# Optimization experiments

Measured on AMD Instinct MI355X. Metric: run time of the kernel, lower is better.

Reference implementation:

```python
import jax, jax.numpy as jnp
import numpy as np

DIM = 1024
EPS = 1e-5


def setup_inputs() -> dict:
    key = jax.random.key(0)
    ks = jax.random.split(key, 7)
    C = DIM
    x = jax.random.normal(ks[0], (4, 4096, C), dtype=jnp.float32)
    norm_w = jnp.ones((C,), dtype=jnp.float32)
    norm_b = jnp.zeros((C,), dtype=jnp.float32)
    s = 1.0 / np.sqrt(C)
    qkv_w = jax.random.uniform(ks[1], (3 * C, C), dtype=jnp.float32, minval=-s, maxval=s)
    qkv_b = jax.random.uniform(ks[2], (3 * C,), dtype=jnp.float32, minval=-s, maxval=s)
    proj_w = jax.random.uniform(ks[3], (C, C), dtype=jnp.float32, minval=-s, maxval=s)
    proj_b = jax.random.uniform(ks[4], (C,), dtype=jnp.float32, minval=-s, maxval=s)
    return {"x": x, "norm_w": norm_w, "norm_b": norm_b, "qkv_w": qkv_w,
            "qkv_b": qkv_b, "proj_w": proj_w, "proj_b": proj_b}


def _layernorm(x, w, b):
    mu = jnp.mean(x, axis=-1, keepdims=True)
    var = jnp.mean(jnp.square(x - mu), axis=-1, keepdims=True)
    return (x - mu) * jax.lax.rsqrt(var + EPS) * w + b


def reference(x, norm_w, norm_b, qkv_w, qkv_b, proj_w, proj_b):
    B, T, C = x.shape
    residual = x
    h = _layernorm(x, norm_w, norm_b)
    qkv = jnp.einsum('btc,oc->bto', h, qkv_w) + qkv_b  # [B,T,3C]
    q, k, v = qkv[..., :C], qkv[..., C:2 * C], qkv[..., 2 * C:]
    attn = jnp.einsum('btc,bsc->bts', q, k) / jnp.sqrt(jnp.float32(C))  # raw QK^T, no softmax
    o = jnp.einsum('bts,bsc->btc', attn, v)
    o = jnp.einsum('btc,oc->bto', o, proj_w) + proj_b
    return residual + o  # dropout is identity in eval mode
```

## Files before the change

kernel.cpp:

```cpp
#include <hip/hip_runtime.h>

typedef _Float16 f16;
typedef _Float16 f16x4 __attribute__((ext_vector_type(4)));
typedef _Float16 f16x8 __attribute__((ext_vector_type(8)));
typedef float f32x4 __attribute__((ext_vector_type(4)));

#define AS1 __attribute__((address_space(1)))
#define AS3 __attribute__((address_space(3)))

__device__ __forceinline__ void gl_lds16(const f16* g, f16* l) {
  __builtin_amdgcn_global_load_lds((const AS1 void*)g, (AS3 void*)l, 16, 0, 0);
}

__global__ __launch_bounds__(256) void ln_kernel(const float* __restrict__ x,
                                                 const float* __restrict__ gw,
                                                 const float* __restrict__ gb,
                                                 f16* __restrict__ H) {
  const int wv = threadIdx.x >> 6, lane = threadIdx.x & 63;
  const long row = (long)blockIdx.x * 4 + wv;
  const float* xr = x + row * 1024;
  float4 v[4];
  float s = 0.f, s2 = 0.f;
#pragma unroll
  for (int j = 0; j < 4; ++j) {
    v[j] = ((const float4*)xr)[lane + 64 * j];
    s  += v[j].x + v[j].y + v[j].z + v[j].w;
    s2 += v[j].x * v[j].x + v[j].y * v[j].y + v[j].z * v[j].z + v[j].w * v[j].w;
  }
#pragma unroll
  for (int off = 32; off > 0; off >>= 1) {
    s  += __shfl_xor(s, off);
    s2 += __shfl_xor(s2, off);
  }
  const float mu = s * (1.0f / 1024.0f);
  const float rstd = rsqrtf(s2 * (1.0f / 1024.0f) - mu * mu + 1e-5f);
#pragma unroll
  for (int j = 0; j < 4; ++j) {
    const float4 w4 = ((const float4*)gw)[lane + 64 * j];
    const float4 b4 = ((const float4*)gb)[lane + 64 * j];
    f16x4 h;
    h[0] = (f16)((v[j].x - mu) * rstd * w4.x + b4.x);
    h[1] = (f16)((v[j].y - mu) * rstd * w4.y + b4.y);
    h[2] = (f16)((v[j].z - mu) * rstd * w4.z + b4.z);
    h[3] = (f16)((v[j].w - mu) * rstd * w4.w + b4.w);
    *(f16x4*)(H + row * 1024 + (lane + 64 * j) * 4) = h;
  }
}

__global__ __launch_bounds__(256) void transpose_cs_kernel(const f16* __restrict__ H,
                                                           f16* __restrict__ Ht,
                                                           float* __restrict__ hs) {
  __shared__ f16 tile[64][68];
  __shared__ float csum[4][64];
  const int b = blockIdx.z;
  const long Hb  = (long)b * 4096 * 1024;
  const long Htb = (long)b * 1024 * 4096;
  const int t0 = blockIdx.y * 64, c0 = blockIdx.x * 64;
  const int tid = threadIdx.x;
  const int r = tid >> 2, g0 = tid & 3;
#pragma unroll
  for (int i = 0; i < 4; ++i) {
    const int g = g0 + i * 4;
    f16x4 v = *(const f16x4*)(H + Hb + (long)(t0 + r) * 1024 + c0 + g * 4);
    *(f16x4*)&tile[r][g * 4] = v;
  }
  __syncthreads();
  {
    const int cl = tid & 63, rg = tid >> 6;
    float s = 0.f;
#pragma unroll
    for (int rr = 0; rr < 16; ++rr) s += (float)tile[rg * 16 + rr][cl];
    csum[rg][cl] = s;
  }
#pragma unroll
  for (int i = 0; i < 4; ++i) {
    const int g = g0 + i * 4;
    f16x4 v;
    v[0] = tile[g * 4 + 0][r];
    v[1] = tile[g * 4 + 1][r];
    v[2] = tile[g * 4 + 2][r];
    v[3] = tile[g * 4 + 3][r];
    *(f16x4*)(Ht + Htb + (long)(c0 + r) * 4096 + t0 + g * 4) = v;
  }
  __syncthreads();
  if (tid < 64)
    atomicAdd(&hs[b * 1024 + c0 + tid],
              csum[0][tid] + csum[1][tid] + csum[2][tid] + csum[3][tid]);
}

__global__ __launch_bounds__(256) void transcast4(const float* __restrict__ qkv_w,
                                                  const float* __restrict__ proj_w,
                                                  f16* __restrict__ WT3,
                                                  f16* __restrict__ Wh,
                                                  f16* __restrict__ Ph) {
  const int z = blockIdx.z;
  __shared__ f16 tile[64][68];
  const int r0 = blockIdx.y * 64, c0 = blockIdx.x * 64;
  const int tid = threadIdx.x;
  const int r = tid >> 2, g0 = tid & 3;
  if (z == 3) {
#pragma unroll
    for (int i = 0; i < 4; ++i) {
      const int g = g0 + i * 4;
      float4 v = *(const float4*)(proj_w + (long)(r0 + r) * 1024 + c0 + g * 4);
      f16x4 h; h[0]=(f16)v.x; h[1]=(f16)v.y; h[2]=(f16)v.z; h[3]=(f16)v.w;
      *(f16x4*)(Ph + (long)(r0 + r) * 1024 + c0 + g * 4) = h;
    }
    return;
  }
  const float* W = qkv_w + (long)z * 1048576;
  f16* WT = WT3 + (long)z * 1048576;
#pragma unroll
  for (int i = 0; i < 4; ++i) {
    const int g = g0 + i * 4;
    float4 v = *(const float4*)(W + (long)(r0 + r) * 1024 + c0 + g * 4);
    f16x4 h; h[0]=(f16)v.x; h[1]=(f16)v.y; h[2]=(f16)v.z; h[3]=(f16)v.w;
    *(f16x4*)&tile[r][g * 4] = h;
    if (z >= 1)
      *(f16x4*)(Wh + (long)z * 1048576 + (long)(r0 + r) * 1024 + c0 + g * 4) = h;
  }
  __syncthreads();
#pragma unroll
  for (int i = 0; i < 4; ++i) {
    const int g = g0 + i * 4;
    f16x4 v;
    v[0] = tile[g * 4 + 0][r];
    v[1] = tile[g * 4 + 1][r];
    v[2] = tile[g * 4 + 2][r];
    v[3] = tile[g * 4 + 3][r];
    *(f16x4*)(WT + (long)(c0 + r) * 1024 + r0 + g * 4) = v;
  }
}

__device__ __forceinline__ float dot1024(const f16* __restrict__ row,
                                         const float* __restrict__ v) {
  const int lane = threadIdx.x & 63;
  float s = 0.f;
#pragma unroll
  for (int j = 0; j < 2; ++j) {
    const int d = (lane + 64 * j) * 8;
    f16x8 a = *(const f16x8*)(row + d);
    float4 h0 = *(const float4*)(v + d);
    float4 h1 = *(const float4*)(v + d + 4);
    s += (float)a[0] * h0.x + (float)a[1] * h0.y + (float)a[2] * h0.z + (float)a[3] * h0.w
       + (float)a[4] * h1.x + (float)a[5] * h1.y + (float)a[6] * h1.z + (float)a[7] * h1.w;
  }
#pragma unroll
  for (int off = 32; off > 0; off >>= 1) s += __shfl_down(s, off);
  return s;
}

__device__ __forceinline__ float dotf1024(const float* __restrict__ a,
                                          const float* __restrict__ v) {
  const int lane = threadIdx.x & 63;
  float s = 0.f;
#pragma unroll
  for (int j = 0; j < 4; ++j) {
    const int d = (lane + 64 * j) * 4;
    float4 x = *(const float4*)(a + d);
    float4 q = *(const float4*)(v + d);
    s += x.x * q.x + x.y * q.y + x.z * q.z + x.w * q.w;
  }
#pragma unroll
  for (int off = 32; off > 0; off >>= 1) s += __shfl_down(s, off);
  return s;
}

__global__ void gemv3a(const f16* __restrict__ WT3, const f16* __restrict__ Ph,
                       const float* __restrict__ qkv_b, float* __restrict__ ayd,
                       float* __restrict__ scal) {
  if (blockIdx.x == 3072) {
    float s = dotf1024(qkv_b + 1024, qkv_b);
    if ((threadIdx.x & 63) == 0) scal[4] = s;
    return;
  }
  const int which = blockIdx.x >> 10, m = blockIdx.x & 1023;
  const f16* row;
  const float* v;
  if (which == 0)      { row = WT3 + (long)m * 1024;            v = qkv_b + 1024; }
  else if (which == 1) { row = WT3 + 1048576 + (long)m * 1024;  v = qkv_b; }
  else                 { row = Ph + (long)m * 1024;             v = qkv_b + 2048; }
  float s = dot1024(row, v);
  if ((threadIdx.x & 63) == 0) ayd[which * 1024 + m] = s;
}

__global__ void gemv_uw2(const f16* __restrict__ Wh, const float* __restrict__ hs,
                         const float* __restrict__ ayd,
                         float* __restrict__ wvec, float* __restrict__ scal) {
  const int bid = blockIdx.x;
  if (bid >= 4096) {
    const int b = bid - 4096;
    float s = dotf1024(hs + b * 1024, ayd + 1024);
    if ((threadIdx.x & 63) == 0) scal[b] = s;
    return;
  }
  const int b = bid >> 10, i = bid & 1023;
  float s = dot1024(Wh + (long)(2048 + i) * 1024, hs + b * 1024);
  if ((threadIdx.x & 63) == 0) wvec[b * 1024 + i] = s;
}

__global__ void gemv3b(const f16* __restrict__ U, const f16* __restrict__ PWv,
                       const f16* __restrict__ Gh, const float* __restrict__ hs,
                       const float* __restrict__ ayd, float* __restrict__ efz) {
  const int sel = blockIdx.x >> 12, r = blockIdx.x & 4095;
  const int b = r >> 10, m = r & 1023;
  const f16* row;
  const float* v;
  if (sel == 0)      { row = U + (long)m * 1024;                       v = hs + b * 1024; }
  else if (sel == 1) { row = PWv + (long)m * 1024;                     v = hs + b * 1024; }
  else               { row = Gh + (long)b * 1048576 + (long)m * 1024;  v = ayd + 1024; }
  float s = dot1024(row, v);
  if ((threadIdx.x & 63) == 0) efz[sel * 4096 + r] = s;
}

__global__ void gemvW(const f16* __restrict__ Wh, const float* __restrict__ efz,
                      const float* __restrict__ qkv_b, const float* __restrict__ scal,
                      const float* __restrict__ wvec, float* __restrict__ w1) {
  const int b = blockIdx.x >> 10, i = blockIdx.x & 1023;
  float s = dot1024(Wh + (long)(2048 + i) * 1024, efz + 8192 + b * 1024);
  if ((threadIdx.x & 63) == 0) {
    const float bv = qkv_b[2048 + i];
    w1[b * 1024 + i] = (s + bv * scal[b] + scal[4] * (wvec[b * 1024 + i] + 4096.f * bv)) * 0.03125f;
  }
}

__global__ void gemvC2(const f16* __restrict__ Ph, const float* __restrict__ w1,
                       const float* __restrict__ proj_b, float* __restrict__ c2) {
  const int b = blockIdx.x >> 10, c = blockIdx.x & 1023;
  float s = dot1024(Ph + (long)c * 1024, w1 + b * 1024);
  if ((threadIdx.x & 63) == 0) c2[b * 1024 + c] = s + proj_b[c];
}

#define GP64_COMMON()                                        \
  const int tid = threadIdx.x;                               \
  const int wave = tid >> 6, lane = tid & 63;                \
  const int lr = lane & 15, lk = lane >> 4;                  \
  const int srow = tid >> 3;                                 \
  const int slc  = (tid & 7) ^ (srow & 7);                   \
  const int kc0 = ((lk) ^ (lr & 7)) * 8;                     \
  const int kc1 = ((4 + lk) ^ (lr & 7)) * 8;

#define GEMM_WAIT8(NBUF_, r_)                                               \
  do {                                                                      \
    if constexpr (NBUF_ == 3) {                                             \
      if ((r_) >= 2)      asm volatile("s_waitcnt vmcnt(16)" ::: "memory"); \
      else if ((r_) == 1) asm volatile("s_waitcnt vmcnt(8)" ::: "memory");  \
      else                asm volatile("s_waitcnt vmcnt(0)" ::: "memory");  \
    } else {                                                                \
      if ((r_) >= 1)      asm volatile("s_waitcnt vmcnt(8)" ::: "memory");  \
      else                asm volatile("s_waitcnt vmcnt(0)" ::: "memory");  \
    }                                                                       \
  } while (0)

#define COMP64_HALF(asb_, bsb_, kc_)                                             \
  do {                                                                           \
    const f16* asb = (asb_);                                                     \
    const f16* bsb = (bsb_);                                                     \
    f16x8 af[4], bf[4];                                                          \
    _Pragma("unroll")                                                            \
    for (int mi = 0; mi < 4; ++mi)                                               \
      af[mi] = *(const f16x8*)(asb + (wm * 64 + mi * 16 + lr) * 64 + (kc_));     \
    _Pragma("unroll")                                                            \
    for (int ni = 0; ni < 4; ++ni)                                               \
      bf[ni] = *(const f16x8*)(bsb + (wn * 64 + ni * 16 + lr) * 64 + (kc_));     \
    _Pragma("unroll")                                                            \
    for (int mi = 0; mi < 4; ++mi)                                               \
      _Pragma("unroll")                                                          \
      for (int ni = 0; ni < 4; ++ni)                                             \
        acc[mi][ni] = __builtin_amdgcn_mfma_f32_16x16x32_f16(af[mi], bf[ni],     \
                                                             acc[mi][ni], 0, 0, 0); \
  } while (0)

#define GEMM_BODY_LOOP(NBUF_, NT_, STAGEM)                       \
  do {                                                           \
    if constexpr (NBUF_ == 3) {                                  \
      STAGEM(0, 0); STAGEM(1, 1);                                \
      int cur = 0, stg = 2;                                      \
      for (int t = 0; t < (NT_); ++t) {                          \
        if (t + 2 < (NT_)) STAGEM(stg, t + 2);                   \
        GEMM_WAIT8(3, (NT_) - 1 - t);                            \
        asm volatile("s_barrier" ::: "memory");                  \
        __builtin_amdgcn_s_setprio(1);                           \
        COMP64_HALF(&As[cur][0], &Bs[cur][0], kc0);              \
        COMP64_HALF(&As[cur][0], &Bs[cur][0], kc1);              \
        __builtin_amdgcn_s_setprio(0);                           \
        asm volatile("s_waitcnt lgkmcnt(0)" ::: "memory");       \
        asm volatile("s_barrier" ::: "memory");                  \
        cur = (cur + 1 == 3) ? 0 : cur + 1;                      \
        stg = (stg + 1 == 3) ? 0 : stg + 1;                      \
      }                                                          \
    } else {                                                     \
      STAGEM(0, 0);                                              \
      int cur = 0;                                               \
      for (int t = 0; t < (NT_); ++t) {                          \
        if (t + 1 < (NT_)) STAGEM(cur ^ 1, t + 1);               \
        GEMM_WAIT8(2, (NT_) - 1 - t);                            \
        asm volatile("s_barrier" ::: "memory");                  \
        __builtin_amdgcn_s_setprio(1);                           \
        COMP64_HALF(&As[cur][0], &Bs[cur][0], kc0);              \
        COMP64_HALF(&As[cur][0], &Bs[cur][0], kc1);              \
        __builtin_amdgcn_s_setprio(0);                           \
        asm volatile("s_waitcnt lgkmcnt(0)" ::: "memory");       \
        asm volatile("s_barrier" ::: "memory");                  \
        cur ^= 1;                                                \
      }                                                          \
    }                                                            \
  } while (0)

template <int MODE>
__global__ __launch_bounds__(256) void gemm128(
    const f16* __restrict__ A, const f16* __restrict__ B, int K,
    long sA, long sB, long sC,
    f16* __restrict__ Ch,
    const float* __restrict__ dvec, const float* __restrict__ evec,
    const float* __restrict__ fvec, const float* __restrict__ avec) {
  const int b = blockIdx.z;
  A += (long)b * sA;
  B += (long)b * sB;
  const int nx = blockIdx.y & 7;
  const int ny = blockIdx.x;

  GP64_COMMON();
  const int wm = wave >> 1, wn = wave & 1;

  __shared__ __align__(16) f16 As[3][8192];
  __shared__ __align__(16) f16 Bs[3][8192];

  const long aoffs = (long)(ny * 128 + srow) * K + slc * 8;
  const long boffs = (long)(nx * 128 + srow) * K + slc * 8;

  f32x4 zero = {0.f, 0.f, 0.f, 0.f};
  f32x4 acc[4][4];
#pragma unroll
  for (int mi = 0; mi < 4; ++mi)
#pragma unroll
    for (int ni = 0; ni < 4; ++ni) acc[mi][ni] = zero;

#define STAGE(buf, kt)                                                              \
  do {                                                                              \
    f16* asb = &As[buf][0];                                                         \
    f16* bsb = &Bs[buf][0];                                                         \
    _Pragma("unroll")                                                               \
    for (int q = 0; q < 4; ++q) {                                                   \
      gl_lds16(A + aoffs + (long)q * 32 * K + (kt) * 64, asb + q * 2048 + tid * 8); \
      gl_lds16(B + boffs + (long)q * 32 * K + (kt) * 64, bsb + q * 2048 + tid * 8); \
    }                                                                               \
  } while (0)

  const int nt = K >> 6;
  GEMM_BODY_LOOP(3, nt, STAGE);
#undef STAGE

  const long cb = (long)b * sC;
  const int m0 = ny * 128 + wm * 64;
  const int n0 = nx * 128 + wn * 64;
#pragma unroll
  for (int mi = 0; mi < 4; ++mi)
#pragma unroll
    for (int ni = 0; ni < 4; ++ni)
#pragma unroll
      for (int j = 0; j < 4; ++j) {
        const int gm = m0 + mi * 16 + lk * 4 + j;
        const int gn = n0 + ni * 16 + lr;
        float val = acc[mi][ni][j];
        if constexpr (MODE == 0) {
          Ch[cb + (long)gm * 1024 + gn] = (f16)val;
        } else {
          const float dm = dvec[gm];
          const float fm = fvec[b * 1024 + gm];
          const float en = evec[b * 1024 + gn];
          const float an = avec[gn];
          val = (val + dm * en + (fm + 4096.f * dm) * an) * 0.03125f;
          Ch[cb + (long)gm * 1024 + gn] = (f16)val;
        }
      }
}

__global__ __launch_bounds__(256) void gemmGUV(const f16* __restrict__ Ht,
                                               const f16* __restrict__ WT3,
                                               const f16* __restrict__ Ph,
                                               f16* __restrict__ part,
                                               f16* __restrict__ U,
                                               f16* __restrict__ PWv) {
  GP64_COMMON();
  const int wm = wave >> 1, wn = wave & 1;

  __shared__ __align__(16) f16 As[2][8192];
  __shared__ __align__(16) f16 Bs[2][8192];

  const int bid = blockIdx.x;
  const f16 *Ab, *Bb;
  long rs;
  int tileid = 0, zz = 0, selt = 0;
  if (bid < 576) {
    tileid = bid % 36;
    zz = bid / 36;
    const int b = zz & 3, ks4 = zz >> 2;
    int ti = 0, trem = tileid;
    while (trem >= 8 - ti) { trem -= 8 - ti; ++ti; }
    const int tj = ti + trem;
    const f16* Hb = Ht + (long)b * 4194304;
    rs = 4096;
    Ab = Hb + (long)(ti * 128 + srow) * 4096 + (long)ks4 * 1024 + slc * 8;
    Bb = Hb + (long)(tj * 128 + srow) * 4096 + (long)ks4 * 1024 + slc * 8;
  } else {
    const int u = bid - 576;
    selt = (u >> 6) + 1;
    const int t = u & 63;
    const int ny = t >> 3, nxx = t & 7;
    const f16* A0 = (selt == 2) ? Ph : WT3;
    const f16* B0 = (selt == 2) ? (WT3 + 2097152) : (WT3 + 1048576);
    rs = 1024;
    Ab = A0 + (long)(ny * 128 + srow) * 1024 + slc * 8;
    Bb = B0 + (long)(nxx * 128 + srow) * 1024 + slc * 8;
  }

  f32x4 zero = {0.f, 0.f, 0.f, 0.f};
  f32x4 acc[4][4];
#pragma unroll
  for (int mi = 0; mi < 4; ++mi)
#pragma unroll
    for (int ni = 0; ni < 4; ++ni) acc[mi][ni] = zero;

#define STAGE(buf, kt)                                                            \
  do {                                                                            \
    f16* asb = &As[buf][0];                                                       \
    f16* bsb = &Bs[buf][0];                                                       \
    _Pragma("unroll")                                                             \
    for (int q = 0; q < 4; ++q) {                                                 \
      gl_lds16(Ab + (long)q * 32 * rs + (kt) * 64, asb + q * 2048 + tid * 8);     \
      gl_lds16(Bb + (long)q * 32 * rs + (kt) * 64, bsb + q * 2048 + tid * 8);     \
    }                                                                             \
  } while (0)

  GEMM_BODY_LOOP(2, 16, STAGE);
#undef STAGE

  if (selt == 0) {
    f16* P = part + ((long)zz * 36 + tileid) * 16384;
#pragma unroll
    for (int mi = 0; mi < 4; ++mi)
#pragma unroll
      for (int ni = 0; ni < 4; ++ni)
#pragma unroll
        for (int j = 0; j < 4; ++j) {
          const int gm = wm * 64 + mi * 16 + lk * 4 + j;
          const int gn = wn * 64 + ni * 16 + lr;
          P[gm * 128 + gn] = (f16)acc[mi][ni][j];
        }
  } else {
    const int u = bid - 576;
    const int t = u & 63;
    const int ny = t >> 3, nxx = t & 7;
    f16* C = (selt == 2) ? PWv : U;
    const int m0 = ny * 128 + wm * 64;
    const int n0 = nxx * 128 + wn * 64;
#pragma unroll
    for (int mi = 0; mi < 4; ++mi)
#pragma unroll
      for (int ni = 0; ni < 4; ++ni)
#pragma unroll
        for (int j = 0; j < 4; ++j) {
          const int gm = m0 + mi * 16 + lk * 4 + j;
          const int gn = n0 + ni * 16 + lr;
          C[(long)gm * 1024 + gn] = (f16)acc[mi][ni][j];
        }
  }
}

__global__ __launch_bounds__(512) void gemm256f(
    const f16* __restrict__ A,
    const f16* __restrict__ Bw,
    const float* __restrict__ resid,
    const float* __restrict__ c2v,
    float* __restrict__ outF) {
  const int lin = blockIdx.y * 4 + blockIdx.x;
  const int xcd = lin & 7, slot = lin >> 3;
  const int ny = xcd * 8 + (slot >> 2);
  const int nx = slot & 3;
  const int bb = ny >> 4;

  GP64_COMMON();
  const int wm = wave >> 2, wn = wave & 3;

  __shared__ __align__(16) f16 As[2][16384];
  __shared__ __align__(16) f16 Bs[2][16384];

  const f16* Ab = A + (long)ny * 262144;
  const f16* Bb = Bw + (long)bb * 1048576 + (long)nx * 262144;
  const long offs = (long)srow * 1024 + slc * 8;

  f32x4 zero = {0.f, 0.f, 0.f, 0.f};
  f32x4 acc[8][4];
#pragma unroll
  for (int mi = 0; mi < 8; ++mi)
#pragma unroll
    for (int ni = 0; ni < 4; ++ni) acc[mi][ni] = zero;

#define STAGE(buf, kt)                                                             \
  do {                                                                             \
    f16* asb = &As[buf][0];                                                        \
    f16* bsb = &Bs[buf][0];                                                        \
    _Pragma("unroll")                                                              \
    for (int q = 0; q < 4; ++q) {                                                  \
      gl_lds16(Ab + offs + (long)q * 65536 + (kt) * 64, asb + q * 4096 + tid * 8); \
      gl_lds16(Bb + offs + (long)q * 65536 + (kt) * 64, bsb + q * 4096 + tid * 8); \
    }                                                                              \
  } while (0)

  const int nt = 16;
  STAGE(0, 0);
  int cur = 0;
  for (int t = 0; t < nt; ++t) {
    if (t + 1 < nt) STAGE(cur ^ 1, t + 1);
    GEMM_WAIT8(2, nt - 1 - t);
    asm volatile("s_barrier" ::: "memory");
    __builtin_amdgcn_s_setprio(1);
#pragma unroll
    for (int ks = 0; ks < 2; ++ks) {
      const int kc = ks ? kc1 : kc0;
      const f16* asb = &As[cur][0];
      const f16* bsb = &Bs[cur][0];
      f16x8 af[8], bf[4];
#pragma unroll
      for (int mi = 0; mi < 8; ++mi)
        af[mi] = *(const f16x8*)(asb + (wm * 128 + mi * 16 + lr) * 64 + kc);
#pragma unroll
      for (int ni = 0; ni < 4; ++ni)
        bf[ni] = *(const f16x8*)(bsb + (wn * 64 + ni * 16 + lr) * 64 + kc);
#pragma unroll
      for (int mi = 0; mi < 8; ++mi)
#pragma unroll
        for (int ni = 0; ni < 4; ++ni)
          acc[mi][ni] = __builtin_amdgcn_mfma_f32_16x16x32_f16(af[mi], bf[ni],
                                                               acc[mi][ni], 0, 0, 0);
    }
    __builtin_amdgcn_s_setprio(0);
    asm volatile("s_waitcnt lgkmcnt(0)" ::: "memory");
    asm volatile("s_barrier" ::: "memory");
    cur ^= 1;
  }
#undef STAGE

  float* weps = ((float*)&As[0][0]) + wave * 1088;
  const int m0 = ny * 256 + wm * 128;
  const int n0 = nx * 256 + wn * 64;
  const int err = lane >> 3;
  const int ecc = (lane & 7) * 4;
  float4 cc2[2];
#pragma unroll
  for (int q = 0; q < 2; ++q)
    cc2[q] = *(const float4*)&c2v[bb * 1024 + n0 + ecc + 32 * q];

  float4 rb0[4], rb1[4];

#define RESLD(DST, MI)                                                            \
  do {                                                                            \
    _Pragma("unroll")                                                             \
    for (int h = 0; h < 2; ++h)                                                   \
      _Pragma("unroll")                                                           \
      for (int q = 0; q < 2; ++q)                                                 \
        DST[h * 2 + q] = *(const float4*)&resid[                                  \
            (long)(m0 + (MI) * 16 + err + 8 * h) * 1024 + n0 + ecc + 32 * q];     \
  } while (0)

#define EPI(MI, CUR, NXT, LASTP)                                                  \
  do {                                                                            \
    _Pragma("unroll")                                                             \
    for (int ni = 0; ni < 4; ++ni)                                                \
      _Pragma("unroll")                                                           \
      for (int j = 0; j < 4; ++j)                                                 \
        weps[(lk * 4 + j) * 68 + ni * 16 + lr] = acc[MI][ni][j];                  \
    if (!(LASTP)) RESLD(NXT, (MI) + 1);                                           \
    asm volatile("s_waitcnt lgkmcnt(0)" ::: "memory");                            \
    _Pragma("unroll")                                                             \
    for (int h = 0; h < 2; ++h)                                                   \
      _Pragma("unroll")                                                           \
      for (int q = 0; q < 2; ++q) {                                               \
        const int rr = err + 8 * h;                                               \
        const int cc = ecc + 32 * q;                                              \
        float4 o = *(const float4*)&weps[rr * 68 + cc];                           \
        const long gbase = (long)(m0 + (MI) * 16 + rr) * 1024 + n0 + cc;          \
        const float4 rv = CUR[h * 2 + q];                                         \
        float4 ov;                                                               \
        ov.x = o.x + rv.x + cc2[q].x;                                             \
        ov.y = o.y + rv.y + cc2[q].y;                                             \
        ov.z = o.z + rv.z + cc2[q].z;                                             \
        ov.w = o.w + rv.w + cc2[q].w;                                             \
        *(float4*)&outF[gbase] = ov;                                              \
      }                                                                           \
  } while (0)

  RESLD(rb0, 0);
  EPI(0, rb0, rb1, 0);
  EPI(1, rb1, rb0, 0);
  EPI(2, rb0, rb1, 0);
  EPI(3, rb1, rb0, 0);
  EPI(4, rb0, rb1, 0);
  EPI(5, rb1, rb0, 0);
  EPI(6, rb0, rb1, 0);
  EPI(7, rb1, rb0, 1);
#undef RESLD
#undef EPI
}

__global__ __launch_bounds__(256) void treduce(const f16* __restrict__ part,
                                               f16* __restrict__ Gh) {
  const int tileid = blockIdx.x, b = blockIdx.y;
  int ti = 0, trem = tileid;
  while (trem >= 8 - ti) { trem -= 8 - ti; ++ti; }
  const int tj = ti + trem;
  __shared__ f16 tl[128][132];
  const int tid = threadIdx.x;
  f16* Gb = Gh + (long)b * 1048576;
  const long pbase = ((long)b * 36 + tileid) * 16384;
#pragma unroll
  for (int it = 0; it < 16; ++it) {
    const int e = it * 1024 + tid * 4;
    const int r = e >> 7, c = e & 127;
    f16x4 p0 = *(const f16x4*)(part + pbase + e);
    f16x4 p1 = *(const f16x4*)(part + pbase + 2359296 + e);
    f16x4 p2 = *(const f16x4*)(part + pbase + 4718592 + e);
    f16x4 p3 = *(const f16x4*)(part + pbase + 7077888 + e);
    f16x4 sv;
#pragma unroll
    for (int j = 0; j < 4; ++j)
      sv[j] = (f16)((float)p0[j] + (float)p1[j] + (float)p2[j] + (float)p3[j]);
    *(f16x4*)(Gb + (long)(ti * 128 + r) * 1024 + tj * 128 + c) = sv;
    *(f16x4*)&tl[r][c] = sv;
  }
  if (ti != tj) {
    __syncthreads();
#pragma unroll
    for (int it = 0; it < 16; ++it) {
      const int e = it * 1024 + tid * 4;
      const int r = e >> 7, c = e & 127;
      f16x4 v;
      v[0] = tl[c + 0][r];
      v[1] = tl[c + 1][r];
      v[2] = tl[c + 2][r];
      v[3] = tl[c + 3][r];
      *(f16x4*)(Gb + (long)(tj * 128 + r) * 1024 + ti * 128 + c) = v;
    }
  }
}

extern "C" void kernel_launch(void* const* d_in, const int* in_sizes, int n_in,
                              void* d_out, int out_size, void* d_ws, size_t ws_size,
                              hipStream_t stream) {
  const float* x      = (const float*)d_in[0];
  const float* norm_w = (const float*)d_in[1];
  const float* norm_b = (const float*)d_in[2];
  const float* qkv_w  = (const float*)d_in[3];
  const float* qkv_b  = (const float*)d_in[4];
  const float* proj_w = (const float*)d_in[5];
  const float* proj_b = (const float*)d_in[6];
  float* out = (float*)d_out;
  char* ws = (char*)d_ws;

  const size_t OFF_H    = 0;
  const size_t OFF_HT   = 33554432;
  const size_t OFF_T1   = 33554432;
  const size_t OFF_T2   = 41943040;
  const size_t OFF_WH   = 67108864;
  const size_t OFF_PH   = 73400320;
  const size_t OFF_WT3  = 75497472;
  const size_t OFF_U    = 81788928;
  const size_t OFF_PWV  = 83886080;
  const size_t OFF_GH   = 85983232;
  const size_t OFF_PART = 94371840;
  const size_t OFF_HS   = 115343360;
  const size_t OFF_WVEC = 115376128;
  const size_t OFF_AYD  = 115392512;
  const size_t OFF_SCAL = 115404800;
  const size_t OFF_EFZ  = 115405824;
  const size_t OFF_W1   = 115454976;
  const size_t OFF_C2   = 115471360;

  f16* H    = (f16*)(ws + OFF_H);
  f16* Ht   = (f16*)(ws + OFF_HT);
  f16* T1   = (f16*)(ws + OFF_T1);
  f16* T2   = (f16*)(ws + OFF_T2);
  f16* Wh   = (f16*)(ws + OFF_WH);
  f16* Ph   = (f16*)(ws + OFF_PH);
  f16* WT3  = (f16*)(ws + OFF_WT3);
  f16* U    = (f16*)(ws + OFF_U);
  f16* PWv  = (f16*)(ws + OFF_PWV);
  f16* Gh   = (f16*)(ws + OFF_GH);
  f16* part = (f16*)(ws + OFF_PART);
  float* hs   = (float*)(ws + OFF_HS);
  float* wvec = (float*)(ws + OFF_WVEC);
  float* ayd  = (float*)(ws + OFF_AYD);
  float* scal = (float*)(ws + OFF_SCAL);
  float* efz  = (float*)(ws + OFF_EFZ);
  float* w1   = (float*)(ws + OFF_W1);
  float* c2v  = (float*)(ws + OFF_C2);

  transcast4<<<dim3(16, 16, 4), 256, 0, stream>>>(qkv_w, proj_w, WT3, Wh, Ph);
  gemv3a<<<dim3(3073), 64, 0, stream>>>(WT3, Ph, qkv_b, ayd, scal);

  ln_kernel<<<dim3(4096), 256, 0, stream>>>(x, norm_w, norm_b, H);
  hipMemsetAsync(ws + OFF_HS, 0, 16384, stream);
  transpose_cs_kernel<<<dim3(16, 64, 4), 256, 0, stream>>>(H, Ht, hs);
  gemv_uw2<<<dim3(4100), 64, 0, stream>>>(Wh, hs, ayd, wvec, scal);

  gemmGUV<<<dim3(704), 256, 0, stream>>>(Ht, WT3, Ph, part, U, PWv);
  treduce<<<dim3(36, 4), 256, 0, stream>>>(part, Gh);

  gemm128<0><<<dim3(8, 8, 4), 256, 0, stream>>>(U, Gh, 1024, 0L, 1048576L, 1048576L,
      T1, nullptr, nullptr, nullptr, nullptr);

  gemv3b<<<dim3(12288), 64, 0, stream>>>(U, PWv, Gh, hs, ayd, efz);
  gemvW<<<dim3(4096), 64, 0, stream>>>(Wh, efz, qkv_b, scal, wvec, w1);
  gemvC2<<<dim3(4096), 64, 0, stream>>>(Ph, w1, proj_b, c2v);

  gemm128<1><<<dim3(8, 8, 4), 256, 0, stream>>>(PWv, T1, 1024, 0L, 1048576L, 1048576L,
      T2, ayd + 2048, efz, efz + 4096, ayd);

  gemm256f<<<dim3(4, 64), 512, 0, stream>>>(H, T2, x, c2v, out);
}
```

Baseline: 208.7 us.

## Fold bias-correction GEMVs via PWv, split final GEMM MFMA phases

The bias-correction chain of three GEMVs (wvec through Wh, w1 through Wh, c2 through Ph) is replaced by one GEMV over the precomputed PWv product plus existing efz terms. The small scal dot products move into gemv3b, which removes two kernel launches and about two matrix-vector passes over 1024x1024 weights. The final gemm256f inner loop now splits the 8 M-fragments into two halves, each with its own LDS wait, priority raise and barrier. Its epilogue also drops the double-buffered residual prefetch in favour of a simpler loop. The extra barriers and the lost residual prefetch could cost time in the large final GEMM.

```diff
diff --git a/kernel.cpp b/kernel.cpp
--- a/kernel.cpp
+++ b/kernel.cpp
@@ -184,24 +184,16 @@
   if ((threadIdx.x & 63) == 0) ayd[which * 1024 + m] = s;
 }
 
-__global__ void gemv_uw2(const f16* __restrict__ Wh, const float* __restrict__ hs,
-                         const float* __restrict__ ayd,
-                         float* __restrict__ wvec, float* __restrict__ scal) {
-  const int bid = blockIdx.x;
-  if (bid >= 4096) {
-    const int b = bid - 4096;
+__global__ void gemv3b(const f16* __restrict__ U, const f16* __restrict__ PWv,
+                       const f16* __restrict__ Gh, const float* __restrict__ hs,
+                       const float* __restrict__ ayd, float* __restrict__ efz,
+                       float* __restrict__ scal) {
+  if (blockIdx.x >= 12288) {
+    const int b = blockIdx.x - 12288;
     float s = dotf1024(hs + b * 1024, ayd + 1024);
     if ((threadIdx.x & 63) == 0) scal[b] = s;
     return;
   }
-  const int b = bid >> 10, i = bid & 1023;
-  float s = dot1024(Wh + (long)(2048 + i) * 1024, hs + b * 1024);
-  if ((threadIdx.x & 63) == 0) wvec[b * 1024 + i] = s;
-}
-
-__global__ void gemv3b(const f16* __restrict__ U, const f16* __restrict__ PWv,
-                       const f16* __restrict__ Gh, const float* __restrict__ hs,
-                       const float* __restrict__ ayd, float* __restrict__ efz) {
   const int sel = blockIdx.x >> 12, r = blockIdx.x & 4095;
   const int b = r >> 10, m = r & 1023;
   const f16* row;
@@ -213,22 +205,16 @@
   if ((threadIdx.x & 63) == 0) efz[sel * 4096 + r] = s;
 }
 
-__global__ void gemvW(const f16* __restrict__ Wh, const float* __restrict__ efz,
-                      const float* __restrict__ qkv_b, const float* __restrict__ scal,
-                      const float* __restrict__ wvec, float* __restrict__ w1) {
-  const int b = blockIdx.x >> 10, i = blockIdx.x & 1023;
-  float s = dot1024(Wh + (long)(2048 + i) * 1024, efz + 8192 + b * 1024);
+__global__ void gemvC2n(const f16* __restrict__ PWv, const float* __restrict__ efz,
+                        const float* __restrict__ ayd, const float* __restrict__ scal,
+                        const float* __restrict__ proj_b, float* __restrict__ c2) {
+  const int b = blockIdx.x >> 10, c = blockIdx.x & 1023;
+  float s = dot1024(PWv + (long)c * 1024, efz + 8192 + b * 1024);
   if ((threadIdx.x & 63) == 0) {
-    const float bv = qkv_b[2048 + i];
-    w1[b * 1024 + i] = (s + bv * scal[b] + scal[4] * (wvec[b * 1024 + i] + 4096.f * bv)) * 0.03125f;
-  }
-}
-
-__global__ void gemvC2(const f16* __restrict__ Ph, const float* __restrict__ w1,
-                       const float* __restrict__ proj_b, float* __restrict__ c2) {
-  const int b = blockIdx.x >> 10, c = blockIdx.x & 1023;
-  float s = dot1024(Ph + (long)c * 1024, w1 + b * 1024);
-  if ((threadIdx.x & 63) == 0) c2[b * 1024 + c] = s + proj_b[c];
+    const float d = ayd[2048 + c];
+    c2[b * 1024 + c] = (s + d * scal[b] + scal[4] * (efz[4096 + b * 1024 + c] + 4096.f * d))
+                         * 0.03125f + proj_b[c];
+  }
 }
 
 #define GP64_COMMON()                                        \
@@ -515,29 +501,42 @@
     if (t + 1 < nt) STAGE(cur ^ 1, t + 1);
     GEMM_WAIT8(2, nt - 1 - t);
     asm volatile("s_barrier" ::: "memory");
-    __builtin_amdgcn_s_setprio(1);
+    const f16* asb = &As[cur][0];
+    const f16* bsb = &Bs[cur][0];
 #pragma unroll
     for (int ks = 0; ks < 2; ++ks) {
       const int kc = ks ? kc1 : kc0;
-      const f16* asb = &As[cur][0];
-      const f16* bsb = &Bs[cur][0];
-      f16x8 af[8], bf[4];
-#pragma unroll
-      for (int mi = 0; mi < 8; ++mi)
-        af[mi] = *(const f16x8*)(asb + (wm * 128 + mi * 16 + lr) * 64 + kc);
+      f16x8 bf[4], af[4];
 #pragma unroll
       for (int ni = 0; ni < 4; ++ni)
         bf[ni] = *(const f16x8*)(bsb + (wn * 64 + ni * 16 + lr) * 64 + kc);
 #pragma unroll
-      for (int mi = 0; mi < 8; ++mi)
+      for (int mi = 0; mi < 4; ++mi)
+        af[mi] = *(const f16x8*)(asb + (wm * 128 + mi * 16 + lr) * 64 + kc);
+      asm volatile("s_waitcnt lgkmcnt(0)" ::: "memory");
+      __builtin_amdgcn_s_setprio(1);
+#pragma unroll
+      for (int mi = 0; mi < 4; ++mi)
 #pragma unroll
         for (int ni = 0; ni < 4; ++ni)
           acc[mi][ni] = __builtin_amdgcn_mfma_f32_16x16x32_f16(af[mi], bf[ni],
                                                                acc[mi][ni], 0, 0, 0);
+      __builtin_amdgcn_s_setprio(0);
+      asm volatile("s_barrier" ::: "memory");
+#pragma unroll
+      for (int mi = 0; mi < 4; ++mi)
+        af[mi] = *(const f16x8*)(asb + (wm * 128 + (mi + 4) * 16 + lr) * 64 + kc);
+      asm volatile("s_waitcnt lgkmcnt(0)" ::: "memory");
+      __builtin_amdgcn_s_setprio(1);
+#pragma unroll
+      for (int mi = 0; mi < 4; ++mi)
+#pragma unroll
+        for (int ni = 0; ni < 4; ++ni)
+          acc[mi + 4][ni] = __builtin_amdgcn_mfma_f32_16x16x32_f16(af[mi], bf[ni],
+                                                                   acc[mi + 4][ni], 0, 0, 0);
+      __builtin_amdgcn_s_setprio(0);
+      asm volatile("s_barrier" ::: "memory");
     }
-    __builtin_amdgcn_s_setprio(0);
-    asm volatile("s_waitcnt lgkmcnt(0)" ::: "memory");
-    asm volatile("s_barrier" ::: "memory");
     cur ^= 1;
   }
 #undef STAGE
@@ -552,56 +551,31 @@
   for (int q = 0; q < 2; ++q)
     cc2[q] = *(const float4*)&c2v[bb * 1024 + n0 + ecc + 32 * q];
 
-  float4 rb0[4], rb1[4];
-
-#define RESLD(DST, MI)                                                            \
-  do {                                                                            \
-    _Pragma("unroll")                                                             \
-    for (int h = 0; h < 2; ++h)                                                   \
-      _Pragma("unroll")                                                           \
-      for (int q = 0; q < 2; ++q)                                                 \
-        DST[h * 2 + q] = *(const float4*)&resid[                                  \
-            (long)(m0 + (MI) * 16 + err + 8 * h) * 1024 + n0 + ecc + 32 * q];     \
-  } while (0)
-
-#define EPI(MI, CUR, NXT, LASTP)                                                  \
-  do {                                                                            \
-    _Pragma("unroll")                                                             \
-    for (int ni = 0; ni < 4; ++ni)                                                \
-      _Pragma("unroll")                                                           \
-      for (int j = 0; j < 4; ++j)                                                 \
-        weps[(lk * 4 + j) * 68 + ni * 16 + lr] = acc[MI][ni][j];                  \
-    if (!(LASTP)) RESLD(NXT, (MI) + 1);                                           \
-    asm volatile("s_waitcnt lgkmcnt(0)" ::: "memory");                            \
-    _Pragma("unroll")                                                             \
-    for (int h = 0; h < 2; ++h)                                                   \
-      _Pragma("unroll")                                                           \
-      for (int q = 0; q < 2; ++q) {                                               \
-        const int rr = err + 8 * h;                                               \
-        const int cc = ecc + 32 * q;                                              \
-        float4 o = *(const float4*)&weps[rr * 68 + cc];                           \
-        const long gbase = (long)(m0 + (MI) * 16 + rr) * 1024 + n0 + cc;          \
-        const float4 rv = CUR[h * 2 + q];                                         \
-        float4 ov;                                                               \
-        ov.x = o.x + rv.x + cc2[q].x;                                             \
-        ov.y = o.y + rv.y + cc2[q].y;                                             \
-        ov.z = o.z + rv.z + cc2[q].z;                                             \
-        ov.w = o.w + rv.w + cc2[q].w;                                             \
-        *(float4*)&outF[gbase] = ov;                                              \
-      }                                                                           \
-  } while (0)
-
-  RESLD(rb0, 0);
-  EPI(0, rb0, rb1, 0);
-  EPI(1, rb1, rb0, 0);
-  EPI(2, rb0, rb1, 0);
-  EPI(3, rb1, rb0, 0);
-  EPI(4, rb0, rb1, 0);
-  EPI(5, rb1, rb0, 0);
-  EPI(6, rb0, rb1, 0);
-  EPI(7, rb1, rb0, 1);
-#undef RESLD
-#undef EPI
+#pragma unroll
+  for (int mi = 0; mi < 8; ++mi) {
+#pragma unroll
+    for (int ni = 0; ni < 4; ++ni)
+#pragma unroll
+      for (int j = 0; j < 4; ++j)
+        weps[(lk * 4 + j) * 68 + ni * 16 + lr] = acc[mi][ni][j];
+    asm volatile("s_waitcnt lgkmcnt(0)" ::: "memory");
+#pragma unroll
+    for (int h = 0; h < 2; ++h)
+#pragma unroll
+      for (int q = 0; q < 2; ++q) {
+        const int rr = err + 8 * h;
+        const int cc = ecc + 32 * q;
+        float4 o = *(const float4*)&weps[rr * 68 + cc];
+        const long gbase = (long)(m0 + mi * 16 + rr) * 1024 + n0 + cc;
+        const float4 rv = *(const float4*)&resid[gbase];
+        float4 ov;
+        ov.x = o.x + rv.x + cc2[q].x;
+        ov.y = o.y + rv.y + cc2[q].y;
+        ov.z = o.z + rv.z + cc2[q].z;
+        ov.w = o.w + rv.w + cc2[q].w;
+        *(float4*)&outF[gbase] = ov;
+      }
+  }
 }
 
 __global__ __launch_bounds__(256) void treduce(const f16* __restrict__ part,
@@ -670,11 +644,9 @@
   const size_t OFF_GH   = 85983232;
   const size_t OFF_PART = 94371840;
   const size_t OFF_HS   = 115343360;
-  const size_t OFF_WVEC = 115376128;
   const size_t OFF_AYD  = 115392512;
   const size_t OFF_SCAL = 115404800;
   const size_t OFF_EFZ  = 115405824;
-  const size_t OFF_W1   = 115454976;
   const size_t OFF_C2   = 115471360;
 
   f16* H    = (f16*)(ws + OFF_H);
@@ -689,11 +661,9 @@
   f16* Gh   = (f16*)(ws + OFF_GH);
   f16* part = (f16*)(ws + OFF_PART);
   float* hs   = (float*)(ws + OFF_HS);
-  float* wvec = (float*)(ws + OFF_WVEC);
   float* ayd  = (float*)(ws + OFF_AYD);
   float* scal = (float*)(ws + OFF_SCAL);
   float* efz  = (float*)(ws + OFF_EFZ);
-  float* w1   = (float*)(ws + OFF_W1);
   float* c2v  = (float*)(ws + OFF_C2);
 
   transcast4<<<dim3(16, 16, 4), 256, 0, stream>>>(qkv_w, proj_w, WT3, Wh, Ph);
@@ -702,18 +672,15 @@
   ln_kernel<<<dim3(4096), 256, 0, stream>>>(x, norm_w, norm_b, H);
   hipMemsetAsync(ws + OFF_HS, 0, 16384, stream);
   transpose_cs_kernel<<<dim3(16, 64, 4), 256, 0, stream>>>(H, Ht, hs);
-  gemv_uw2<<<dim3(4100), 64, 0, stream>>>(Wh, hs, ayd, wvec, scal);
 
   gemmGUV<<<dim3(704), 256, 0, stream>>>(Ht, WT3, Ph, part, U, PWv);
   treduce<<<dim3(36, 4), 256, 0, stream>>>(part, Gh);
 
+  gemv3b<<<dim3(12292), 64, 0, stream>>>(U, PWv, Gh, hs, ayd, efz, scal);
+  gemvC2n<<<dim3(4096), 64, 0, stream>>>(PWv, efz, ayd, scal, proj_b, c2v);
+
   gemm128<0><<<dim3(8, 8, 4), 256, 0, stream>>>(U, Gh, 1024, 0L, 1048576L, 1048576L,
       T1, nullptr, nullptr, nullptr, nullptr);
-
-  gemv3b<<<dim3(12288), 64, 0, stream>>>(U, PWv, Gh, hs, ayd, efz);
-  gemvW<<<dim3(4096), 64, 0, stream>>>(Wh, efz, qkv_b, scal, wvec, w1);
-  gemvC2<<<dim3(4096), 64, 0, stream>>>(Ph, w1, proj_b, c2v);
-
   gemm128<1><<<dim3(8, 8, 4), 256, 0, stream>>>(PWv, T1, 1024, 0L, 1048576L, 1048576L,
       T2, ayd + 2048, efz, efz + 4096, ayd);
 
```

Measured after the change: 203.6 us. -2.4%, faster.
